# Optimization experiments

Hardware: AMD Instinct MI355X
Metric: run time of the kernel (lower is better)

Reference implementation:

```python
import jax, jax.numpy as jnp
import numpy as np
from jax import lax

B, S, I, H, DELAY = 64, 512, 1024, 1024, 4


def setup_inputs() -> dict:
    key = jax.random.key(0)
    ks = jax.random.split(key, 6)
    scale_ih = 1.0 / np.sqrt(I)
    scale_hh = 1.0 / np.sqrt(H)
    return {
        "inputs": jax.random.normal(ks[0], (B, S, I), dtype=jnp.float32),
        "hidden_state": jax.random.normal(ks[1], (DELAY, B, H), dtype=jnp.float32),
        "Wih": jax.random.normal(ks[2], (H, I), dtype=jnp.float32) * scale_ih,
        "Whh": jax.random.normal(ks[3], (H, H), dtype=jnp.float32) * scale_hh,
        "bih": jax.random.normal(ks[4], (H,), dtype=jnp.float32) * scale_ih,
        "bhh": jax.random.normal(ks[5], (H,), dtype=jnp.float32) * scale_hh,
    }


def reference(inputs, hidden_state, Wih, Whh, bih, bhh):
    # hidden_state: [delay, B, H] deque; each step consumes the oldest state
    # (delay steps back) and appends the new one, per the torch deque logic.
    delay = hidden_state.shape[0]
    hidden_state = hidden_state.reshape(delay, -1, Whh.shape[0])

    def step(h_queue, x_t):
        # x_t: [B, I]; h_queue[0] is the state from `delay` steps ago
        h_new = jnp.tanh(x_t @ Wih.T + bih + h_queue[0] @ Whh.T + bhh)
        h_queue = jnp.concatenate([h_queue[1:], h_new[None]], axis=0)
        return h_queue, h_new

    xs = jnp.swapaxes(inputs, 0, 1)  # [S, B, I]
    h_final, outs = lax.scan(step, hidden_state, xs)
    return jnp.swapaxes(outs, 0, 1), h_final  # [B, S, H], [delay, B, H]
```

## Files before the change

### kernel.cpp

```cpp
#include <hip/hip_runtime.h>

typedef _Float16 half8 __attribute__((ext_vector_type(8)));
typedef _Float16 half4v __attribute__((ext_vector_type(4)));
typedef float f32x4 __attribute__((ext_vector_type(4)));

#define OUT_MAIN 33554432L

#define WS_PRE   0L
#define WS_WIH   67108864L
#define WS_WHH   69206016L
#define WS_HBUF  71303168L
#define WS_BIAS  72351744L
#define WS_CTR   72355840L

__device__ __forceinline__ half8 ic_load16(const _Float16* p) {
  unsigned long long lo = __hip_atomic_load((unsigned long long*)p,
      __ATOMIC_RELAXED, __HIP_MEMORY_SCOPE_AGENT);
  unsigned long long hi = __hip_atomic_load((unsigned long long*)p + 1,
      __ATOMIC_RELAXED, __HIP_MEMORY_SCOPE_AGENT);
  union { unsigned long long u[2]; half8 h; } cv;
  cv.u[0] = lo; cv.u[1] = hi;
  return cv.h;
}

__global__ __launch_bounds__(256) void prep_kernel(
    const float* __restrict__ wih, const float* __restrict__ whh,
    const float* __restrict__ hid, const float* __restrict__ bih,
    const float* __restrict__ bhh,
    _Float16* __restrict__ wihf, _Float16* __restrict__ whhf,
    _Float16* __restrict__ hbuf, float* __restrict__ bias,
    unsigned* __restrict__ ctr) {
  int tid = blockIdx.x * 256 + threadIdx.x;
  int np = gridDim.x * 256;
  for (int i = tid; i < 262144; i += np) {
    float4 v = ((const float4*)wih)[i];
    half4v h; h[0]=(_Float16)v.x; h[1]=(_Float16)v.y; h[2]=(_Float16)v.z; h[3]=(_Float16)v.w;
    ((half4v*)wihf)[i] = h;
  }
  for (int i = tid; i < 262144; i += np) {
    float4 v = ((const float4*)whh)[i];
    half4v h; h[0]=(_Float16)v.x; h[1]=(_Float16)v.y; h[2]=(_Float16)v.z; h[3]=(_Float16)v.w;
    ((half4v*)whhf)[i] = h;
  }
  for (int i = tid; i < 65536; i += np) {
    float4 v = ((const float4*)hid)[i];
    half4v h; h[0]=(_Float16)v.x; h[1]=(_Float16)v.y; h[2]=(_Float16)v.z; h[3]=(_Float16)v.w;
    ((half4v*)hbuf)[i] = h;
  }
  for (int i = tid; i < 1024; i += np) bias[i] = bih[i] + bhh[i];
  if (tid < 8) ctr[tid * 32] = 0u;
}

__global__ __launch_bounds__(256, 2) void gemm_pre(
    const float* __restrict__ x, const _Float16* __restrict__ wih,
    const float* __restrict__ bias, _Float16* __restrict__ pre) {
  __shared__ _Float16 Ash[128 * 64];
  __shared__ _Float16 Bsh[128 * 64];
  int tid = threadIdx.x;
  int lane = tid & 63, wid = tid >> 6;
  int l15 = lane & 15, quad = lane >> 4;
  int mt = blockIdx.x >> 3, nt = blockIdx.x & 7;
  int m0 = mt * 128, n0 = nt * 128;
  int wm = (wid >> 1) * 64, wn = (wid & 1) * 64;
  f32x4 acc[4][4] = {};

  for (int ko = 0; ko < 16; ++ko) {
    int k0 = ko * 64;
#pragma unroll
    for (int p = 0; p < 4; ++p) {
      int s = p * 256 + tid;
      int row = s >> 3;
      int kkh = (s & 7) ^ (row & 7);
      const float* g = x + (long)(m0 + row) * 1024 + k0 + kkh * 8;
      float4 v0 = ((const float4*)g)[0];
      float4 v1 = ((const float4*)g)[1];
      half8 hv;
      hv[0]=(_Float16)v0.x; hv[1]=(_Float16)v0.y; hv[2]=(_Float16)v0.z; hv[3]=(_Float16)v0.w;
      hv[4]=(_Float16)v1.x; hv[5]=(_Float16)v1.y; hv[6]=(_Float16)v1.z; hv[7]=(_Float16)v1.w;
      *(half8*)(Ash + (long)s * 8) = hv;
    }
#pragma unroll
    for (int p = 0; p < 4; ++p) {
      int s = p * 256 + tid;
      int row = s >> 3;
      int kkh = (s & 7) ^ (row & 7);
      const _Float16* g = wih + (long)(n0 + row) * 1024 + k0 + kkh * 8;
      __builtin_amdgcn_global_load_lds(
          (const __attribute__((address_space(1))) void*)g,
          (__attribute__((address_space(3))) void*)(Bsh + (p * 256 + wid * 64) * 8),
          16, 0, 0);
    }
    __syncthreads();
#pragma unroll
    for (int kk = 0; kk < 2; ++kk) {
      half8 af[4], bf[4];
      int kkh = kk * 4 + quad;
#pragma unroll
      for (int i = 0; i < 4; ++i) {
        int ra = wm + i * 16 + l15;
        af[i] = *(const half8*)(Ash + (ra * 8 + (kkh ^ (ra & 7))) * 8);
        int rb = wn + i * 16 + l15;
        bf[i] = *(const half8*)(Bsh + (rb * 8 + (kkh ^ (rb & 7))) * 8);
      }
#pragma unroll
      for (int i = 0; i < 4; ++i)
#pragma unroll
        for (int j = 0; j < 4; ++j)
          acc[i][j] = __builtin_amdgcn_mfma_f32_16x16x32_f16(af[i], bf[j], acc[i][j], 0, 0, 0);
    }
    __syncthreads();
  }
#pragma unroll
  for (int i = 0; i < 4; ++i)
#pragma unroll
    for (int j = 0; j < 4; ++j) {
      int col = n0 + wn + j * 16 + l15;
      float bv = bias[col];
#pragma unroll
      for (int r = 0; r < 4; ++r) {
        int row = m0 + wm + i * 16 + quad * 4 + r;
        pre[(long)row * 1024 + col] = (_Float16)(acc[i][j][r] + bv);
      }
    }
}

__global__ __launch_bounds__(256, 1) void rnn_kernel(
    const _Float16* __restrict__ pre, const _Float16* __restrict__ whhf,
    _Float16* __restrict__ hbuf, unsigned* ctr, float* __restrict__ out) {
  __shared__ _Float16 part[4][128][36];
  const int rg = blockIdx.x & 7, cg = blockIdx.x >> 3;
  const int tid = threadIdx.x;
  const int w = tid >> 6, lane = tid & 63;
  const int l15 = lane & 15, quad = lane >> 4;
  const int q0 = rg * 32, c0 = cg * 128;

  half8 bf[8][8];
#pragma unroll
  for (int kk = 0; kk < 8; ++kk)
#pragma unroll
    for (int j = 0; j < 8; ++j)
      bf[kk][j] = *(const half8*)(whhf + (long)(c0 + j * 16 + l15) * 1024 +
                                  w * 256 + kk * 32 + quad * 8);

  const int oc = (tid & 31) * 4;
  const int orow = (tid >> 5) * 4;
  long obase[4];
  int hoff[4];
#pragma unroll
  for (int r = 0; r < 4; ++r) {
    int q = q0 + orow + r;
    int b = q & 63, rr = q >> 6;
    obase[r] = (long)(b * 512 + rr) * 1024 + c0 + oc;
    hoff[r] = q * 1024 + c0 + oc;
  }
  unsigned* myctr = ctr + rg * 32;
  const int arow = q0 + l15;

  for (int k = 0; k < 128; ++k) {
    const _Float16* hcur = hbuf + (long)(k & 1) * 262144;
    _Float16* hnxt = hbuf + (long)((k + 1) & 1) * 262144;
    half4v pv[4];
#pragma unroll
    for (int r = 0; r < 4; ++r)
      pv[r] = *(const half4v*)(pre + obase[r] + (long)k * 4096);
    const _Float16* ap = hcur + (long)arow * 1024 + w * 256 + quad * 8;
    half8 a0[8], a1[8];
#pragma unroll
    for (int kk = 0; kk < 8; ++kk) {
      a0[kk] = ic_load16(ap + kk * 32);
      a1[kk] = ic_load16(ap + 16 * 1024 + kk * 32);
    }
    f32x4 acc[2][8] = {};
#pragma unroll
    for (int kk = 0; kk < 8; ++kk)
#pragma unroll
      for (int j = 0; j < 8; ++j) {
        acc[0][j] = __builtin_amdgcn_mfma_f32_16x16x32_f16(a0[kk], bf[kk][j], acc[0][j], 0, 0, 0);
        acc[1][j] = __builtin_amdgcn_mfma_f32_16x16x32_f16(a1[kk], bf[kk][j], acc[1][j], 0, 0, 0);
      }
#pragma unroll
    for (int t = 0; t < 2; ++t)
#pragma unroll
      for (int j = 0; j < 8; ++j) {
        half4v hv;
#pragma unroll
        for (int r = 0; r < 4; ++r) hv[r] = (_Float16)acc[t][j][r];
        *(half4v*)&part[w][j * 16 + l15][t * 16 + quad * 4] = hv;
      }
    __syncthreads();
    float z[4][4];
#pragma unroll
    for (int r = 0; r < 4; ++r)
#pragma unroll
      for (int c = 0; c < 4; ++c) z[r][c] = (float)pv[r][c];
#pragma unroll
    for (int w4 = 0; w4 < 4; ++w4)
#pragma unroll
      for (int c = 0; c < 4; ++c) {
        half4v p = *(const half4v*)&part[w4][oc + c][orow];
#pragma unroll
        for (int r = 0; r < 4; ++r) z[r][c] += (float)p[r];
      }
#pragma unroll
    for (int r = 0; r < 4; ++r) {
      f32x4 ov;
      union { _Float16 hh[4]; unsigned long long u; } pk;
#pragma unroll
      for (int c = 0; c < 4; ++c) {
        float e = __expf(2.f * z[r][c]);
        float h = 1.f - 2.f * __builtin_amdgcn_rcpf(e + 1.f);
        ov[c] = h;
        pk.hh[c] = (_Float16)h;
      }
      *(f32x4*)(out + obase[r] + (long)k * 4096) = ov;
      if (k < 127)
        __hip_atomic_store((unsigned long long*)(hnxt + hoff[r]), pk.u,
                           __ATOMIC_RELAXED, __HIP_MEMORY_SCOPE_AGENT);
      else
        *(f32x4*)(out + OUT_MAIN + hoff[r]) = ov;
    }
    if (k < 127) {
      __syncthreads();
      if (tid == 0) {
        __hip_atomic_fetch_add(myctr, 1u, __ATOMIC_RELAXED, __HIP_MEMORY_SCOPE_AGENT);
        unsigned tgt = 8u * (unsigned)(k + 1);
        while (__hip_atomic_load(myctr, __ATOMIC_RELAXED, __HIP_MEMORY_SCOPE_AGENT) < tgt)
          __builtin_amdgcn_s_sleep(1);
      }
      __syncthreads();
    }
  }
}

extern "C" void kernel_launch(void* const* d_in, const int* in_sizes, int n_in,
                              void* d_out, int out_size, void* d_ws, size_t ws_size,
                              hipStream_t stream) {
  const float* x   = (const float*)d_in[0];
  const float* hid = (const float*)d_in[1];
  const float* wih = (const float*)d_in[2];
  const float* whh = (const float*)d_in[3];
  const float* bih = (const float*)d_in[4];
  const float* bhh = (const float*)d_in[5];
  char* ws = (char*)d_ws;
  _Float16* pre  = (_Float16*)(ws + WS_PRE);
  _Float16* wihf = (_Float16*)(ws + WS_WIH);
  _Float16* whhf = (_Float16*)(ws + WS_WHH);
  _Float16* hbuf = (_Float16*)(ws + WS_HBUF);
  float* bias    = (float*)(ws + WS_BIAS);
  unsigned* ctr  = (unsigned*)(ws + WS_CTR);
  float* out     = (float*)d_out;

  hipLaunchKernelGGL(prep_kernel, dim3(256), dim3(256), 0, stream,
                     wih, whh, hid, bih, bhh, wihf, whhf, hbuf, bias, ctr);
  hipLaunchKernelGGL(gemm_pre, dim3(2048), dim3(256), 0, stream, x, wihf, bias, pre);
  hipLaunchKernelGGL(rnn_kernel, dim3(64), dim3(256), 0, stream,
                     pre, whhf, hbuf, ctr, out);
}
```

Measured before the change: 1.150 ms.

## Split recurrent kernel over more blocks with per-block flag barrier and prefetch

Halves the column slice per block (128 to 64 columns) and doubles the grid from 64 to 128 blocks, so each step's recurrent GEMM is spread over more CUs with fewer MFMAs per block. The shared counter barrier is replaced by per-block monotonic flags that 16 threads poll. Partial sums are now kept in fp32 in shared memory, and the next step's precomputed input projection is prefetched while waiting on the barrier. The cost is more blocks joining each step's barrier, scalar 2-byte atomic stores of the hidden state, and uncoalesced scalar output writes.

```diff
diff --git a/kernel.cpp b/kernel.cpp
--- a/kernel.cpp
+++ b/kernel.cpp
@@ -48,7 +48,7 @@
     ((half4v*)hbuf)[i] = h;
   }
   for (int i = tid; i < 1024; i += np) bias[i] = bih[i] + bhh[i];
-  if (tid < 8) ctr[tid * 32] = 0u;
+  for (int i = tid; i < 4096; i += np) ctr[i] = 0u;
 }
 
 __global__ __launch_bounds__(256, 2) void gemm_pre(
@@ -127,42 +127,45 @@
 __global__ __launch_bounds__(256, 1) void rnn_kernel(
     const _Float16* __restrict__ pre, const _Float16* __restrict__ whhf,
     _Float16* __restrict__ hbuf, unsigned* ctr, float* __restrict__ out) {
-  __shared__ _Float16 part[4][128][36];
+  __shared__ float part[4][64][36];
   const int rg = blockIdx.x & 7, cg = blockIdx.x >> 3;
   const int tid = threadIdx.x;
   const int w = tid >> 6, lane = tid & 63;
   const int l15 = lane & 15, quad = lane >> 4;
-  const int q0 = rg * 32, c0 = cg * 128;
-
-  half8 bf[8][8];
+  const int q0 = rg * 32, c0 = cg * 64;
+
+  half8 bf[8][4];
 #pragma unroll
   for (int kk = 0; kk < 8; ++kk)
 #pragma unroll
-    for (int j = 0; j < 8; ++j)
+    for (int j = 0; j < 4; ++j) {
       bf[kk][j] = *(const half8*)(whhf + (long)(c0 + j * 16 + l15) * 1024 +
                                   w * 256 + kk * 32 + quad * 8);
-
-  const int oc = (tid & 31) * 4;
-  const int orow = (tid >> 5) * 4;
-  long obase[4];
-  int hoff[4];
+      asm volatile("" : "+v"(bf[kk][j]));
+    }
+
+  const int cA = tid & 31, orow = (tid >> 5) * 4;
+  long obA[4], obB[4];
+  int hoA[4], hoB[4];
 #pragma unroll
   for (int r = 0; r < 4; ++r) {
-    int q = q0 + orow + r;
-    int b = q & 63, rr = q >> 6;
-    obase[r] = (long)(b * 512 + rr) * 1024 + c0 + oc;
-    hoff[r] = q * 1024 + c0 + oc;
-  }
-  unsigned* myctr = ctr + rg * 32;
+    int qg = q0 + orow + r;
+    int b = qg & 63, ph = qg >> 6;
+    obA[r] = (long)(b * 512 + ph) * 1024 + c0 + cA;
+    obB[r] = obA[r] + 32;
+    hoA[r] = qg * 1024 + c0 + cA;
+    hoB[r] = hoA[r] + 32;
+  }
+  unsigned* flags = ctr + rg * 512;
   const int arow = q0 + l15;
+
+  _Float16 pvA[4], pvB[4];
+#pragma unroll
+  for (int r = 0; r < 4; ++r) { pvA[r] = pre[obA[r]]; pvB[r] = pre[obB[r]]; }
 
   for (int k = 0; k < 128; ++k) {
     const _Float16* hcur = hbuf + (long)(k & 1) * 262144;
     _Float16* hnxt = hbuf + (long)((k + 1) & 1) * 262144;
-    half4v pv[4];
-#pragma unroll
-    for (int r = 0; r < 4; ++r)
-      pv[r] = *(const half4v*)(pre + obase[r] + (long)k * 4096);
     const _Float16* ap = hcur + (long)arow * 1024 + w * 256 + quad * 8;
     half8 a0[8], a1[8];
 #pragma unroll
@@ -170,64 +173,79 @@
       a0[kk] = ic_load16(ap + kk * 32);
       a1[kk] = ic_load16(ap + 16 * 1024 + kk * 32);
     }
-    f32x4 acc[2][8] = {};
+    f32x4 acc[2][4] = {};
 #pragma unroll
     for (int kk = 0; kk < 8; ++kk)
 #pragma unroll
-      for (int j = 0; j < 8; ++j) {
+      for (int j = 0; j < 4; ++j) {
         acc[0][j] = __builtin_amdgcn_mfma_f32_16x16x32_f16(a0[kk], bf[kk][j], acc[0][j], 0, 0, 0);
         acc[1][j] = __builtin_amdgcn_mfma_f32_16x16x32_f16(a1[kk], bf[kk][j], acc[1][j], 0, 0, 0);
       }
 #pragma unroll
     for (int t = 0; t < 2; ++t)
 #pragma unroll
-      for (int j = 0; j < 8; ++j) {
-        half4v hv;
-#pragma unroll
-        for (int r = 0; r < 4; ++r) hv[r] = (_Float16)acc[t][j][r];
-        *(half4v*)&part[w][j * 16 + l15][t * 16 + quad * 4] = hv;
-      }
+      for (int j = 0; j < 4; ++j)
+        *(f32x4*)&part[w][j * 16 + l15][t * 16 + quad * 4] = acc[t][j];
     __syncthreads();
-    float z[4][4];
-#pragma unroll
-    for (int r = 0; r < 4; ++r)
-#pragma unroll
-      for (int c = 0; c < 4; ++c) z[r][c] = (float)pv[r][c];
-#pragma unroll
-    for (int w4 = 0; w4 < 4; ++w4)
-#pragma unroll
-      for (int c = 0; c < 4; ++c) {
-        half4v p = *(const half4v*)&part[w4][oc + c][orow];
-#pragma unroll
-        for (int r = 0; r < 4; ++r) z[r][c] += (float)p[r];
-      }
-#pragma unroll
-    for (int r = 0; r < 4; ++r) {
-      f32x4 ov;
-      union { _Float16 hh[4]; unsigned long long u; } pk;
-#pragma unroll
-      for (int c = 0; c < 4; ++c) {
-        float e = __expf(2.f * z[r][c]);
-        float h = 1.f - 2.f * __builtin_amdgcn_rcpf(e + 1.f);
-        ov[c] = h;
-        pk.hh[c] = (_Float16)h;
-      }
-      *(f32x4*)(out + obase[r] + (long)k * 4096) = ov;
-      if (k < 127)
-        __hip_atomic_store((unsigned long long*)(hnxt + hoff[r]), pk.u,
+    float hA[4], hB[4];
+    {
+      f32x4 zA = {(float)pvA[0], (float)pvA[1], (float)pvA[2], (float)pvA[3]};
+      f32x4 zB = {(float)pvB[0], (float)pvB[1], (float)pvB[2], (float)pvB[3]};
+#pragma unroll
+      for (int w4 = 0; w4 < 4; ++w4) {
+        f32x4 pA = *(const f32x4*)&part[w4][cA][orow];
+        f32x4 pB = *(const f32x4*)&part[w4][cA + 32][orow];
+        zA += pA; zB += pB;
+      }
+#pragma unroll
+      for (int r = 0; r < 4; ++r) {
+        float eA = __expf(2.f * zA[r]);
+        hA[r] = 1.f - 2.f * __builtin_amdgcn_rcpf(eA + 1.f);
+        float eB = __expf(2.f * zB[r]);
+        hB[r] = 1.f - 2.f * __builtin_amdgcn_rcpf(eB + 1.f);
+      }
+    }
+    if (k < 127) {
+#pragma unroll
+      for (int r = 0; r < 4; ++r) {
+        union { _Float16 h; unsigned short u; } ua, ub;
+        ua.h = (_Float16)hA[r]; ub.h = (_Float16)hB[r];
+        __hip_atomic_store((unsigned short*)(hnxt + hoA[r]), ua.u,
                            __ATOMIC_RELAXED, __HIP_MEMORY_SCOPE_AGENT);
-      else
-        *(f32x4*)(out + OUT_MAIN + hoff[r]) = ov;
-    }
-    if (k < 127) {
+        __hip_atomic_store((unsigned short*)(hnxt + hoB[r]), ub.u,
+                           __ATOMIC_RELAXED, __HIP_MEMORY_SCOPE_AGENT);
+      }
       __syncthreads();
-      if (tid == 0) {
-        __hip_atomic_fetch_add(myctr, 1u, __ATOMIC_RELAXED, __HIP_MEMORY_SCOPE_AGENT);
-        unsigned tgt = 8u * (unsigned)(k + 1);
-        while (__hip_atomic_load(myctr, __ATOMIC_RELAXED, __HIP_MEMORY_SCOPE_AGENT) < tgt)
+      if (tid == 0)
+        __hip_atomic_store(&flags[cg * 32], (unsigned)(k + 1),
+                           __ATOMIC_RELAXED, __HIP_MEMORY_SCOPE_AGENT);
+#pragma unroll
+      for (int r = 0; r < 4; ++r) {
+        long ko = (long)k * 4096;
+        out[obA[r] + ko] = hA[r];
+        out[obB[r] + ko] = hB[r];
+      }
+#pragma unroll
+      for (int r = 0; r < 4; ++r) {
+        long ko = (long)(k + 1) * 4096;
+        pvA[r] = pre[obA[r] + ko];
+        pvB[r] = pre[obB[r] + ko];
+      }
+      if (tid < 16) {
+        while (__hip_atomic_load(&flags[tid * 32], __ATOMIC_RELAXED,
+                                 __HIP_MEMORY_SCOPE_AGENT) < (unsigned)(k + 1))
           __builtin_amdgcn_s_sleep(1);
       }
       __syncthreads();
+    } else {
+#pragma unroll
+      for (int r = 0; r < 4; ++r) {
+        long ko = (long)k * 4096;
+        out[obA[r] + ko] = hA[r];
+        out[obB[r] + ko] = hB[r];
+        out[OUT_MAIN + hoA[r]] = hA[r];
+        out[OUT_MAIN + hoB[r]] = hB[r];
+      }
     }
   }
 }
@@ -253,6 +271,6 @@
   hipLaunchKernelGGL(prep_kernel, dim3(256), dim3(256), 0, stream,
                      wih, whh, hid, bih, bhh, wihf, whhf, hbuf, bias, ctr);
   hipLaunchKernelGGL(gemm_pre, dim3(2048), dim3(256), 0, stream, x, wihf, bias, pre);
-  hipLaunchKernelGGL(rnn_kernel, dim3(64), dim3(256), 0, stream,
+  hipLaunchKernelGGL(rnn_kernel, dim3(128), dim3(256), 0, stream,
                      pre, whhf, hbuf, ctr, out);
 }
```

Measured after the change: 974.3 us. 1.18x faster.
